# Kernel tuning notes

Hardware: AMD Instinct MI355X
Metric: run time of the kernel (lower is better)

Reference implementation:

```python
import jax, jax.numpy as jnp
import numpy as np

B, N, DIM_IN, DIM_OUT, CHEB_K, EMBED_DIM = 64, 2048, 64, 64, 3, 10


def setup_inputs() -> dict:
    key = jax.random.key(0)
    k1, k2, k3, k4 = jax.random.split(key, 4)
    x = jax.random.normal(k1, (B, N, DIM_IN), dtype=jnp.float32)
    node_embeddings = jax.random.normal(k2, (N, EMBED_DIM), dtype=jnp.float32)
    # xavier-normal-like init for the pools
    w_std = (2.0 / (EMBED_DIM * CHEB_K * DIM_IN + DIM_OUT)) ** 0.5
    b_std = (2.0 / (EMBED_DIM + DIM_OUT)) ** 0.5
    weights_pool = jax.random.normal(k3, (EMBED_DIM, CHEB_K, DIM_IN, DIM_OUT), dtype=jnp.float32) * w_std
    bias_pool = jax.random.normal(k4, (EMBED_DIM, DIM_OUT), dtype=jnp.float32) * b_std
    return {"x": x, "node_embeddings": node_embeddings,
            "weights_pool": weights_pool, "bias_pool": bias_pool,
            "cheb_k": CHEB_K}


def reference(x, node_embeddings, weights_pool, bias_pool, cheb_k):
    n = node_embeddings.shape[0]
    # adaptive adjacency: softmax(relu(E E^T)) over neighbors
    supports = jax.nn.softmax(jax.nn.relu(node_embeddings @ node_embeddings.T), axis=1)
    # Chebyshev polynomial supports: T0 = I, T1 = A, Tk = 2 A T_{k-1} - T_{k-2}
    support_set = [jnp.eye(n, dtype=supports.dtype), supports]
    for _ in range(2, cheb_k):
        support_set.append(2.0 * supports @ support_set[-1] - support_set[-2])
    supports_k = jnp.stack(support_set, axis=0)  # [K, N, N]
    # per-node weights and bias synthesized from node embeddings
    weights = jnp.einsum('nd,dkio->nkio', node_embeddings, weights_pool)  # [N, K, I, O]
    bias = node_embeddings @ bias_pool                                    # [N, O]
    # graph convolution
    x_g = jnp.einsum('knm,bmc->bnkc', supports_k, x)                      # [B, N, K, I]
    out = jnp.einsum('bnki,nkio->bno', x_g, weights) + bias               # [B, N, O]
    return out
```

## Files before the change

### kernel.cpp

```cpp
#include <hip/hip_runtime.h>

#define NN 2048
#define BB 64
#define CC 64
#define ED 10
#define KK 3
#define JJ (BB * CC)

typedef unsigned short ushort_t;
typedef __attribute__((ext_vector_type(8))) short short8;
typedef __attribute__((ext_vector_type(4))) float f32x4;

typedef const __attribute__((address_space(1))) unsigned* gptr_t;
typedef __attribute__((address_space(3))) unsigned* lptr_t;

static __device__ __forceinline__ ushort_t f2bf(float f) {
    union { float f; unsigned u; } x{f};
    unsigned r = x.u + 0x7FFF + ((x.u >> 16) & 1);
    return (ushort_t)(r >> 16);
}
static __device__ __forceinline__ float bf2f(ushort_t h) {
    union { unsigned u; float f; } x;
    x.u = ((unsigned)h) << 16;
    return x.f;
}

__global__ __launch_bounds__(256) void supports_kernel(const float* __restrict__ E,
                                                       ushort_t* __restrict__ Ab) {
    const int n = blockIdx.x;
    const int tid = threadIdx.x;

    float en[ED];
#pragma unroll
    for (int d = 0; d < ED; ++d) en[d] = E[n * ED + d];

    float sv[NN / 256];
    float lmax = 0.0f;
#pragma unroll
    for (int j = 0; j < NN / 256; ++j) {
        const int m = tid + j * 256;
        const float* Em = E + m * ED;
        float dot = 0.0f;
#pragma unroll
        for (int d = 0; d < ED; ++d) dot += en[d] * Em[d];
        float s = fmaxf(dot, 0.0f);
        sv[j] = s;
        lmax = fmaxf(lmax, s);
    }

    __shared__ float smax[4];
    __shared__ float ssum[4];
#pragma unroll
    for (int off = 32; off > 0; off >>= 1) lmax = fmaxf(lmax, __shfl_down(lmax, off, 64));
    if ((tid & 63) == 0) smax[tid >> 6] = lmax;
    __syncthreads();
    const float bmax = fmaxf(fmaxf(smax[0], smax[1]), fmaxf(smax[2], smax[3]));

    float lsum = 0.0f;
#pragma unroll
    for (int j = 0; j < NN / 256; ++j) {
        sv[j] = __expf(sv[j] - bmax);
        lsum += sv[j];
    }
#pragma unroll
    for (int off = 32; off > 0; off >>= 1) lsum += __shfl_down(lsum, off, 64);
    if ((tid & 63) == 0) ssum[tid >> 6] = lsum;
    __syncthreads();
    const float inv = 1.0f / (ssum[0] + ssum[1] + ssum[2] + ssum[3]);

#pragma unroll
    for (int j = 0; j < NN / 256; ++j) {
        Ab[(size_t)n * NN + tid + j * 256] = f2bf(sv[j] * inv);
    }
}

__global__ __launch_bounds__(256) void transpose_kernel(const float* __restrict__ x,
                                                        ushort_t* __restrict__ xT,
                                                        ushort_t* __restrict__ xN) {
    const int n0 = blockIdx.x * 64;
    const int b = blockIdx.y;
    const int tid = threadIdx.x;

    __shared__ float tb[64][68];

#pragma unroll
    for (int l = 0; l < 4; ++l) {
        const int idx = tid + l * 256;
        const int nn = idx >> 4;
        const int c4 = (idx & 15) << 2;
        const float4 v = *(const float4*)(x + ((size_t)b * NN + n0 + nn) * CC + c4);
        tb[c4 + 0][nn] = v.x;
        tb[c4 + 1][nn] = v.y;
        tb[c4 + 2][nn] = v.z;
        tb[c4 + 3][nn] = v.w;
    }
    __syncthreads();

#pragma unroll
    for (int l = 0; l < 2; ++l) {
        const int idx = tid + l * 256;
        const int c = idx >> 3;
        const int ch = (idx & 7) << 3;
        ushort_t pack[8];
#pragma unroll
        for (int e = 0; e < 8; ++e) pack[e] = f2bf(tb[c][ch + e]);
        *(float4*)(xT + (size_t)(b * 64 + c) * NN + n0 + ch) = *(float4*)pack;
    }
#pragma unroll
    for (int l = 0; l < 2; ++l) {
        const int idx = tid + l * 256;
        const int nn = idx >> 3;
        const int cg = (idx & 7) << 3;
        ushort_t pack[8];
#pragma unroll
        for (int e = 0; e < 8; ++e) pack[e] = f2bf(tb[cg + e][nn]);
        *(float4*)(xN + (size_t)(n0 + nn) * JJ + b * 64 + cg) = *(float4*)pack;
    }
}

__global__ __launch_bounds__(256) void wprep_kernel(const float* __restrict__ Wp,
                                                    ushort_t* __restrict__ WpT) {
    const int dk = blockIdx.x;
    const int tid = threadIdx.x;
    const float* src = Wp + (size_t)dk * CC * CC;

    __shared__ float tb[64][68];

#pragma unroll
    for (int l = 0; l < 4; ++l) {
        const int idx = tid + l * 256;
        const int i = idx >> 4;
        const int o4 = (idx & 15) << 2;
        const float4 v = *(const float4*)(src + i * CC + o4);
        tb[o4 + 0][i] = v.x;
        tb[o4 + 1][i] = v.y;
        tb[o4 + 2][i] = v.z;
        tb[o4 + 3][i] = v.w;
    }
    __syncthreads();

#pragma unroll
    for (int l = 0; l < 2; ++l) {
        const int idx = tid + l * 256;
        const int o = idx >> 3;
        const int ic = (idx & 7) << 3;
        ushort_t pack[8];
#pragma unroll
        for (int e = 0; e < 8; ++e) pack[e] = f2bf(tb[o][ic + e]);
        *(float4*)(WpT + (size_t)dk * CC * CC + o * CC + ic) = *(float4*)pack;
    }
}

template <int MODE>
__global__ __launch_bounds__(256) void gemm_nt(const ushort_t* __restrict__ A,
                                               const ushort_t* __restrict__ Bt,
                                               const ushort_t* __restrict__ Zn,
                                               ushort_t* __restrict__ Ct,
                                               ushort_t* __restrict__ Cn) {
    const int j0 = blockIdx.x * 128;
    const int m0 = blockIdx.y * 128;
    const int tid = threadIdx.x;
    const int lane = tid & 63;
    const int l16 = lane & 15;
    const int quad = lane >> 4;
    const int w = tid >> 6;
    const int wm = (w >> 1) * 64;
    const int wj = (w & 1) * 64;
    const int lr = lane >> 3;
    const int lc = lane & 7;
    const int swz = lc ^ lr;

    __shared__ ushort_t As[128 * 64];
    __shared__ ushort_t Bs[128 * 64];

    f32x4 acc[4][4];
#pragma unroll
    for (int mi = 0; mi < 4; ++mi)
#pragma unroll
        for (int ji = 0; ji < 4; ++ji) acc[mi][ji] = (f32x4){0.f, 0.f, 0.f, 0.f};

    for (int k0 = 0; k0 < NN; k0 += 64) {
#pragma unroll
        for (int inst = 0; inst < 4; ++inst) {
            const int rbase = w * 32 + inst * 8;
            const int row = rbase + lr;
            __builtin_amdgcn_global_load_lds(
                (gptr_t)(A + (size_t)(m0 + row) * NN + k0 + swz * 8),
                (lptr_t)&As[rbase * 64], 16, 0, 0);
            __builtin_amdgcn_global_load_lds(
                (gptr_t)(Bt + (size_t)(j0 + row) * NN + k0 + swz * 8),
                (lptr_t)&Bs[rbase * 64], 16, 0, 0);
        }
        __syncthreads();

#pragma unroll
        for (int ks = 0; ks < 64; ks += 32) {
            const int qb = (ks >> 3) + quad;
            short8 av[4], bv[4];
#pragma unroll
            for (int mi = 0; mi < 4; ++mi) {
                const int rA = wm + mi * 16 + l16;
                av[mi] = *(const short8*)&As[rA * 64 + ((qb ^ (rA & 7)) << 3)];
            }
#pragma unroll
            for (int ji = 0; ji < 4; ++ji) {
                const int rB = wj + ji * 16 + l16;
                bv[ji] = *(const short8*)&Bs[rB * 64 + ((qb ^ (rB & 7)) << 3)];
            }
#pragma unroll
            for (int mi = 0; mi < 4; ++mi)
#pragma unroll
                for (int ji = 0; ji < 4; ++ji)
                    acc[mi][ji] = __builtin_amdgcn_mfma_f32_16x16x32_bf16(
                        av[mi], bv[ji], acc[mi][ji], 0, 0, 0);
        }
        __syncthreads();
    }

#pragma unroll
    for (int mi = 0; mi < 4; ++mi) {
#pragma unroll
        for (int ji = 0; ji < 4; ++ji) {
            const int j = j0 + wj + ji * 16 + l16;
            const int mb = m0 + wm + mi * 16 + quad * 4;
            if (MODE == 0) {
                ushort_t o[4];
#pragma unroll
                for (int r = 0; r < 4; ++r) o[r] = f2bf(acc[mi][ji][r]);
                *(unsigned long long*)(Ct + (size_t)j * NN + mb) = *(unsigned long long*)o;
#pragma unroll
                for (int r = 0; r < 4; ++r) Cn[(size_t)(mb + r) * JJ + j] = o[r];
            } else {
#pragma unroll
                for (int r = 0; r < 4; ++r) {
                    const float z = bf2f(Zn[(size_t)(mb + r) * JJ + j]);
                    Cn[(size_t)(mb + r) * JJ + j] = f2bf(2.0f * acc[mi][ji][r] - z);
                }
            }
        }
    }
}

#define XLD 200
__global__ __launch_bounds__(256) void out_kernel(const float* __restrict__ E,
                                                  const ushort_t* __restrict__ WpT,
                                                  const float* __restrict__ bp,
                                                  const ushort_t* __restrict__ xN,
                                                  const ushort_t* __restrict__ y1N,
                                                  const ushort_t* __restrict__ y2N,
                                                  float* __restrict__ out) {
    const int n = blockIdx.x;
    const int tid = threadIdx.x;

    __shared__ ushort_t xg[BB * XLD];
    __shared__ ushort_t Wt[CC * XLD];
    __shared__ float en_s[ED];
    __shared__ float bias_s[CC];

    if (tid < ED) en_s[tid] = E[n * ED + tid];
    __syncthreads();

    float en[ED];
#pragma unroll
    for (int d = 0; d < ED; ++d) en[d] = en_s[d];

    if (tid < CC) {
        float bsum = 0.0f;
#pragma unroll
        for (int d = 0; d < ED; ++d) bsum += en[d] * bp[d * CC + tid];
        bias_s[tid] = bsum;
    }

#pragma unroll
    for (int k = 0; k < KK; ++k) {
        const ushort_t* src = (k == 0) ? xN : (k == 1) ? y1N : y2N;
        const float4* srow = (const float4*)(src + (size_t)n * JJ);
        for (int idx = tid; idx < JJ / 8; idx += 256) {
            *(float4*)&xg[(idx >> 3) * XLD + k * 64 + ((idx & 7) << 3)] = srow[idx];
        }
    }

    for (int t = tid; t < CC * 24; t += 256) {
        const int o = t / 24;
        const int kc = t % 24;
        const int k = kc >> 3;
        const int ic = (kc & 7) << 3;
        float s[8];
#pragma unroll
        for (int e = 0; e < 8; ++e) s[e] = 0.0f;
#pragma unroll
        for (int d = 0; d < ED; ++d) {
            const float4 wv4 = *(const float4*)(WpT + ((size_t)(d * KK + k) * CC + o) * CC + ic);
            const ushort_t* wp = (const ushort_t*)&wv4;
#pragma unroll
            for (int e = 0; e < 8; ++e) s[e] += en[d] * bf2f(wp[e]);
        }
        ushort_t pack[8];
#pragma unroll
        for (int e = 0; e < 8; ++e) pack[e] = f2bf(s[e]);
        *(float4*)&Wt[o * XLD + k * 64 + ic] = *(float4*)pack;
    }
    __syncthreads();

    const int lane = tid & 63;
    const int l16 = lane & 15;
    const int quad = lane >> 4;
    const int bm = (tid >> 6) * 16;

    f32x4 acc[4];
#pragma unroll
    for (int ji = 0; ji < 4; ++ji) acc[ji] = (f32x4){0.f, 0.f, 0.f, 0.f};

#pragma unroll
    for (int kc = 0; kc < 6; ++kc) {
        const short8 av = *(const short8*)&xg[(bm + l16) * XLD + kc * 32 + quad * 8];
#pragma unroll
        for (int ji = 0; ji < 4; ++ji) {
            const short8 bv = *(const short8*)&Wt[(ji * 16 + l16) * XLD + kc * 32 + quad * 8];
            acc[ji] = __builtin_amdgcn_mfma_f32_16x16x32_bf16(av, bv, acc[ji], 0, 0, 0);
        }
    }

#pragma unroll
    for (int ji = 0; ji < 4; ++ji) {
        const int o = ji * 16 + l16;
        const float bo = bias_s[o];
#pragma unroll
        for (int r = 0; r < 4; ++r) {
            const int b = bm + quad * 4 + r;
            out[((size_t)b * NN + n) * CC + o] = acc[ji][r] + bo;
        }
    }
}
#undef XLD

extern "C" void kernel_launch(void* const* d_in, const int* in_sizes, int n_in,
                              void* d_out, int out_size, void* d_ws, size_t ws_size,
                              hipStream_t stream) {
    const float* x  = (const float*)d_in[0];
    const float* E  = (const float*)d_in[1];
    const float* Wp = (const float*)d_in[2];
    const float* bp = (const float*)d_in[3];

    ushort_t* Ab  = (ushort_t*)d_ws;
    ushort_t* xT  = Ab + (size_t)NN * NN;
    ushort_t* xN  = xT + (size_t)JJ * NN;
    ushort_t* y1T = xN + (size_t)NN * JJ;
    ushort_t* y1N = y1T + (size_t)JJ * NN;
    ushort_t* y2N = y1N + (size_t)NN * JJ;
    ushort_t* WpT = y2N + (size_t)NN * JJ;
    float* out = (float*)d_out;

    supports_kernel<<<NN, 256, 0, stream>>>(E, Ab);
    transpose_kernel<<<dim3(NN / 64, BB), 256, 0, stream>>>(x, xT, xN);
    wprep_kernel<<<ED * KK, 256, 0, stream>>>(Wp, WpT);
    gemm_nt<0><<<dim3(JJ / 128, NN / 128), 256, 0, stream>>>(Ab, xT, nullptr, y1T, y1N);
    gemm_nt<1><<<dim3(JJ / 128, NN / 128), 256, 0, stream>>>(Ab, y1T, xN, nullptr, y2N);
    out_kernel<<<NN, 256, 0, stream>>>(E, WpT, bp, xN, y1N, y2N, out);
}
```

Measured before the change: 221.5 us.

## Double-buffer GEMM LDS tiles and precompute per-node weights in separate kernel

The Chebyshev GEMM now double-buffers its A/B tiles in LDS, issuing the next k-tile's global_load_lds before computing on the current one, with a single barrier per iteration. The per-node weight synthesis moves out of out_kernel into a new wall_kernel that handles 4 nodes per block, reusing each loaded weight-pool vector across those nodes. Results are written into the now-free Ab workspace region, processed in two halves to fit. This doubles GEMM LDS use, which may lower occupancy, and adds two launches plus a round trip through global memory for the synthesized weights.

```diff
diff --git a/kernel.cpp b/kernel.cpp
--- a/kernel.cpp
+++ b/kernel.cpp
@@ -6,6 +6,7 @@
 #define ED 10
 #define KK 3
 #define JJ (BB * CC)
+#define WROW (KK * CC * CC)
 
 typedef unsigned short ushort_t;
 typedef __attribute__((ext_vector_type(8))) short short8;
@@ -151,6 +152,51 @@
     }
 }
 
+#define WNPB 4
+__global__ __launch_bounds__(256) void wall_kernel(const float* __restrict__ E,
+                                                   const ushort_t* __restrict__ WpT,
+                                                   ushort_t* __restrict__ Wall,
+                                                   int n_base) {
+    const int n0 = n_base + blockIdx.x * WNPB;
+    const int tid = threadIdx.x;
+
+    __shared__ float es[WNPB][ED];
+    if (tid < WNPB * ED) es[tid / ED][tid % ED] = E[(size_t)(n0 + tid / ED) * ED + tid % ED];
+    __syncthreads();
+
+#pragma unroll
+    for (int c = 0; c < 6; ++c) {
+        const int t = c * 256 + tid;
+        const int k = t >> 9;
+        const int off = (t & 511) << 3;
+        float vals[ED][8];
+#pragma unroll
+        for (int d = 0; d < ED; ++d) {
+            const float4 p = *(const float4*)(WpT + (size_t)(d * KK + k) * CC * CC + off);
+            const ushort_t* pp = (const ushort_t*)&p;
+#pragma unroll
+            for (int e = 0; e < 8; ++e) vals[d][e] = bf2f(pp[e]);
+        }
+#pragma unroll
+        for (int nl = 0; nl < WNPB; ++nl) {
+            float acc[8];
+#pragma unroll
+            for (int e = 0; e < 8; ++e) acc[e] = 0.0f;
+#pragma unroll
+            for (int d = 0; d < ED; ++d) {
+                const float ed = es[nl][d];
+#pragma unroll
+                for (int e = 0; e < 8; ++e) acc[e] += ed * vals[d][e];
+            }
+            ushort_t pk[8];
+#pragma unroll
+            for (int e = 0; e < 8; ++e) pk[e] = f2bf(acc[e]);
+            *(float4*)(Wall + (size_t)(blockIdx.x * WNPB + nl) * WROW + (size_t)t * 8) =
+                *(float4*)pk;
+        }
+    }
+}
+
 template <int MODE>
 __global__ __launch_bounds__(256) void gemm_nt(const ushort_t* __restrict__ A,
                                                const ushort_t* __restrict__ Bt,
@@ -170,8 +216,8 @@
     const int lc = lane & 7;
     const int swz = lc ^ lr;
 
-    __shared__ ushort_t As[128 * 64];
-    __shared__ ushort_t Bs[128 * 64];
+    __shared__ ushort_t As[2][128 * 64];
+    __shared__ ushort_t Bs[2][128 * 64];
 
     f32x4 acc[4][4];
 #pragma unroll
@@ -179,19 +225,36 @@
 #pragma unroll
         for (int ji = 0; ji < 4; ++ji) acc[mi][ji] = (f32x4){0.f, 0.f, 0.f, 0.f};
 
-    for (int k0 = 0; k0 < NN; k0 += 64) {
-#pragma unroll
-        for (int inst = 0; inst < 4; ++inst) {
-            const int rbase = w * 32 + inst * 8;
-            const int row = rbase + lr;
-            __builtin_amdgcn_global_load_lds(
-                (gptr_t)(A + (size_t)(m0 + row) * NN + k0 + swz * 8),
-                (lptr_t)&As[rbase * 64], 16, 0, 0);
-            __builtin_amdgcn_global_load_lds(
-                (gptr_t)(Bt + (size_t)(j0 + row) * NN + k0 + swz * 8),
-                (lptr_t)&Bs[rbase * 64], 16, 0, 0);
-        }
+#pragma unroll
+    for (int inst = 0; inst < 4; ++inst) {
+        const int rbase = w * 32 + inst * 8;
+        const int row = rbase + lr;
+        __builtin_amdgcn_global_load_lds(
+            (gptr_t)(A + (size_t)(m0 + row) * NN + swz * 8),
+            (lptr_t)&As[0][rbase * 64], 16, 0, 0);
+        __builtin_amdgcn_global_load_lds(
+            (gptr_t)(Bt + (size_t)(j0 + row) * NN + swz * 8),
+            (lptr_t)&Bs[0][rbase * 64], 16, 0, 0);
+    }
+
+    for (int it = 0; it < NN / 64; ++it) {
+        const int cur = it & 1;
         __syncthreads();
+
+        if (it + 1 < NN / 64) {
+            const int k0 = (it + 1) * 64;
+#pragma unroll
+            for (int inst = 0; inst < 4; ++inst) {
+                const int rbase = w * 32 + inst * 8;
+                const int row = rbase + lr;
+                __builtin_amdgcn_global_load_lds(
+                    (gptr_t)(A + (size_t)(m0 + row) * NN + k0 + swz * 8),
+                    (lptr_t)&As[1 - cur][rbase * 64], 16, 0, 0);
+                __builtin_amdgcn_global_load_lds(
+                    (gptr_t)(Bt + (size_t)(j0 + row) * NN + k0 + swz * 8),
+                    (lptr_t)&Bs[1 - cur][rbase * 64], 16, 0, 0);
+            }
+        }
 
 #pragma unroll
         for (int ks = 0; ks < 64; ks += 32) {
@@ -200,12 +263,12 @@
 #pragma unroll
             for (int mi = 0; mi < 4; ++mi) {
                 const int rA = wm + mi * 16 + l16;
-                av[mi] = *(const short8*)&As[rA * 64 + ((qb ^ (rA & 7)) << 3)];
+                av[mi] = *(const short8*)&As[cur][rA * 64 + ((qb ^ (rA & 7)) << 3)];
             }
 #pragma unroll
             for (int ji = 0; ji < 4; ++ji) {
                 const int rB = wj + ji * 16 + l16;
-                bv[ji] = *(const short8*)&Bs[rB * 64 + ((qb ^ (rB & 7)) << 3)];
+                bv[ji] = *(const short8*)&Bs[cur][rB * 64 + ((qb ^ (rB & 7)) << 3)];
             }
 #pragma unroll
             for (int mi = 0; mi < 4; ++mi)
@@ -214,7 +277,6 @@
                     acc[mi][ji] = __builtin_amdgcn_mfma_f32_16x16x32_bf16(
                         av[mi], bv[ji], acc[mi][ji], 0, 0, 0);
         }
-        __syncthreads();
     }
 
 #pragma unroll
@@ -243,31 +305,24 @@
 
 #define XLD 200
 __global__ __launch_bounds__(256) void out_kernel(const float* __restrict__ E,
-                                                  const ushort_t* __restrict__ WpT,
+                                                  const ushort_t* __restrict__ Wall,
                                                   const float* __restrict__ bp,
                                                   const ushort_t* __restrict__ xN,
                                                   const ushort_t* __restrict__ y1N,
                                                   const ushort_t* __restrict__ y2N,
-                                                  float* __restrict__ out) {
-    const int n = blockIdx.x;
+                                                  float* __restrict__ out,
+                                                  int n_base) {
+    const int n = n_base + blockIdx.x;
     const int tid = threadIdx.x;
 
     __shared__ ushort_t xg[BB * XLD];
     __shared__ ushort_t Wt[CC * XLD];
-    __shared__ float en_s[ED];
     __shared__ float bias_s[CC];
-
-    if (tid < ED) en_s[tid] = E[n * ED + tid];
-    __syncthreads();
-
-    float en[ED];
-#pragma unroll
-    for (int d = 0; d < ED; ++d) en[d] = en_s[d];
 
     if (tid < CC) {
         float bsum = 0.0f;
 #pragma unroll
-        for (int d = 0; d < ED; ++d) bsum += en[d] * bp[d * CC + tid];
+        for (int d = 0; d < ED; ++d) bsum += E[(size_t)n * ED + d] * bp[d * CC + tid];
         bias_s[tid] = bsum;
     }
 
@@ -279,26 +334,14 @@
             *(float4*)&xg[(idx >> 3) * XLD + k * 64 + ((idx & 7) << 3)] = srow[idx];
         }
     }
-
-    for (int t = tid; t < CC * 24; t += 256) {
-        const int o = t / 24;
-        const int kc = t % 24;
-        const int k = kc >> 3;
-        const int ic = (kc & 7) << 3;
-        float s[8];
-#pragma unroll
-        for (int e = 0; e < 8; ++e) s[e] = 0.0f;
-#pragma unroll
-        for (int d = 0; d < ED; ++d) {
-            const float4 wv4 = *(const float4*)(WpT + ((size_t)(d * KK + k) * CC + o) * CC + ic);
-            const ushort_t* wp = (const ushort_t*)&wv4;
-#pragma unroll
-            for (int e = 0; e < 8; ++e) s[e] += en[d] * bf2f(wp[e]);
-        }
-        ushort_t pack[8];
-#pragma unroll
-        for (int e = 0; e < 8; ++e) pack[e] = f2bf(s[e]);
-        *(float4*)&Wt[o * XLD + k * 64 + ic] = *(float4*)pack;
+    {
+        const float4* wrow = (const float4*)(Wall + (size_t)blockIdx.x * WROW);
+        for (int t = tid; t < WROW / 8; t += 256) {
+            const int k = t >> 9;
+            const int o = (t & 511) >> 3;
+            const int ic = (t & 7) << 3;
+            *(float4*)&Wt[o * XLD + k * 64 + ic] = wrow[t];
+        }
     }
     __syncthreads();
 
@@ -342,19 +385,28 @@
     const float* Wp = (const float*)d_in[2];
     const float* bp = (const float*)d_in[3];
 
-    ushort_t* Ab  = (ushort_t*)d_ws;
+    const size_t MB = 1024 * 1024 / 2;
+    ushort_t* base = (ushort_t*)d_ws;
+    ushort_t* WpT  = base;
+    ushort_t* xN   = base + (size_t)(256 * 1024) / 2 * 2;
+    xN  = base + 131072;
+    ushort_t* y1N = xN + (size_t)NN * JJ;
+    ushort_t* y2N = y1N + (size_t)NN * JJ;
+    ushort_t* Ab  = y2N + (size_t)NN * JJ;
     ushort_t* xT  = Ab + (size_t)NN * NN;
-    ushort_t* xN  = xT + (size_t)JJ * NN;
-    ushort_t* y1T = xN + (size_t)NN * JJ;
-    ushort_t* y1N = y1T + (size_t)JJ * NN;
-    ushort_t* y2N = y1N + (size_t)NN * JJ;
-    ushort_t* WpT = y2N + (size_t)NN * JJ;
+    ushort_t* y1T = xT + (size_t)JJ * NN;
+    ushort_t* Wall = Ab;
     float* out = (float*)d_out;
+    (void)MB;
 
     supports_kernel<<<NN, 256, 0, stream>>>(E, Ab);
     transpose_kernel<<<dim3(NN / 64, BB), 256, 0, stream>>>(x, xT, xN);
     wprep_kernel<<<ED * KK, 256, 0, stream>>>(Wp, WpT);
     gemm_nt<0><<<dim3(JJ / 128, NN / 128), 256, 0, stream>>>(Ab, xT, nullptr, y1T, y1N);
     gemm_nt<1><<<dim3(JJ / 128, NN / 128), 256, 0, stream>>>(Ab, y1T, xN, nullptr, y2N);
-    out_kernel<<<NN, 256, 0, stream>>>(E, WpT, bp, xN, y1N, y2N, out);
-}
+    const int NH = NN / 2;
+    wall_kernel<<<NH / WNPB, 256, 0, stream>>>(E, WpT, Wall, 0);
+    out_kernel<<<NH, 256, 0, stream>>>(E, Wall, bp, xN, y1N, y2N, out, 0);
+    wall_kernel<<<NH / WNPB, 256, 0, stream>>>(E, WpT, Wall, NH);
+    out_kernel<<<NH, 256, 0, stream>>>(E, Wall, bp, xN, y1N, y2N, out, NH);
+}
```

Measured after the change: 253.1 us. 1.14x slower.

## Double-buffer GEMM LDS tiles and merge prep kernels into one launch

Applied to the files above, without the earlier changes.

The GEMM main loop now uses two LDS buffers per operand. Global-to-LDS loads for the next K tile are issued before the MFMAs on the current tile, and one barrier per iteration is dropped. The softmax-supports, x transpose and weight-pool prep kernels are merged into a single launch with block-index dispatch, which cuts launch overhead and lets the independent prep work run concurrently. LDS use per GEMM block doubles to 64 KB, which may reduce occupancy. The single barrier per iteration relies on the load-to-LDS wait ordering being correct.

```diff
diff --git a/kernel.cpp b/kernel.cpp
--- a/kernel.cpp
+++ b/kernel.cpp
@@ -25,129 +25,125 @@
     return x.f;
 }
 
-__global__ __launch_bounds__(256) void supports_kernel(const float* __restrict__ E,
-                                                       ushort_t* __restrict__ Ab) {
-    const int n = blockIdx.x;
+__global__ __launch_bounds__(256) void prep_kernel(const float* __restrict__ E,
+                                                   const float* __restrict__ x,
+                                                   const float* __restrict__ Wp,
+                                                   ushort_t* __restrict__ Ab,
+                                                   ushort_t* __restrict__ xT,
+                                                   ushort_t* __restrict__ xN,
+                                                   ushort_t* __restrict__ WpT) {
+    const int bid = blockIdx.x;
     const int tid = threadIdx.x;
 
-    float en[ED];
-#pragma unroll
-    for (int d = 0; d < ED; ++d) en[d] = E[n * ED + d];
-
-    float sv[NN / 256];
-    float lmax = 0.0f;
-#pragma unroll
-    for (int j = 0; j < NN / 256; ++j) {
-        const int m = tid + j * 256;
-        const float* Em = E + m * ED;
-        float dot = 0.0f;
-#pragma unroll
-        for (int d = 0; d < ED; ++d) dot += en[d] * Em[d];
-        float s = fmaxf(dot, 0.0f);
-        sv[j] = s;
-        lmax = fmaxf(lmax, s);
-    }
-
-    __shared__ float smax[4];
-    __shared__ float ssum[4];
-#pragma unroll
-    for (int off = 32; off > 0; off >>= 1) lmax = fmaxf(lmax, __shfl_down(lmax, off, 64));
-    if ((tid & 63) == 0) smax[tid >> 6] = lmax;
-    __syncthreads();
-    const float bmax = fmaxf(fmaxf(smax[0], smax[1]), fmaxf(smax[2], smax[3]));
-
-    float lsum = 0.0f;
-#pragma unroll
-    for (int j = 0; j < NN / 256; ++j) {
-        sv[j] = __expf(sv[j] - bmax);
-        lsum += sv[j];
-    }
-#pragma unroll
-    for (int off = 32; off > 0; off >>= 1) lsum += __shfl_down(lsum, off, 64);
-    if ((tid & 63) == 0) ssum[tid >> 6] = lsum;
-    __syncthreads();
-    const float inv = 1.0f / (ssum[0] + ssum[1] + ssum[2] + ssum[3]);
-
-#pragma unroll
-    for (int j = 0; j < NN / 256; ++j) {
-        Ab[(size_t)n * NN + tid + j * 256] = f2bf(sv[j] * inv);
-    }
-}
-
-__global__ __launch_bounds__(256) void transpose_kernel(const float* __restrict__ x,
-                                                        ushort_t* __restrict__ xT,
-                                                        ushort_t* __restrict__ xN) {
-    const int n0 = blockIdx.x * 64;
-    const int b = blockIdx.y;
-    const int tid = threadIdx.x;
-
     __shared__ float tb[64][68];
-
-#pragma unroll
-    for (int l = 0; l < 4; ++l) {
-        const int idx = tid + l * 256;
-        const int nn = idx >> 4;
-        const int c4 = (idx & 15) << 2;
-        const float4 v = *(const float4*)(x + ((size_t)b * NN + n0 + nn) * CC + c4);
-        tb[c4 + 0][nn] = v.x;
-        tb[c4 + 1][nn] = v.y;
-        tb[c4 + 2][nn] = v.z;
-        tb[c4 + 3][nn] = v.w;
-    }
-    __syncthreads();
-
-#pragma unroll
-    for (int l = 0; l < 2; ++l) {
-        const int idx = tid + l * 256;
-        const int c = idx >> 3;
-        const int ch = (idx & 7) << 3;
-        ushort_t pack[8];
-#pragma unroll
-        for (int e = 0; e < 8; ++e) pack[e] = f2bf(tb[c][ch + e]);
-        *(float4*)(xT + (size_t)(b * 64 + c) * NN + n0 + ch) = *(float4*)pack;
-    }
-#pragma unroll
-    for (int l = 0; l < 2; ++l) {
-        const int idx = tid + l * 256;
-        const int nn = idx >> 3;
-        const int cg = (idx & 7) << 3;
-        ushort_t pack[8];
-#pragma unroll
-        for (int e = 0; e < 8; ++e) pack[e] = f2bf(tb[cg + e][nn]);
-        *(float4*)(xN + (size_t)(n0 + nn) * JJ + b * 64 + cg) = *(float4*)pack;
-    }
-}
-
-__global__ __launch_bounds__(256) void wprep_kernel(const float* __restrict__ Wp,
-                                                    ushort_t* __restrict__ WpT) {
-    const int dk = blockIdx.x;
-    const int tid = threadIdx.x;
-    const float* src = Wp + (size_t)dk * CC * CC;
-
-    __shared__ float tb[64][68];
-
-#pragma unroll
-    for (int l = 0; l < 4; ++l) {
-        const int idx = tid + l * 256;
-        const int i = idx >> 4;
-        const int o4 = (idx & 15) << 2;
-        const float4 v = *(const float4*)(src + i * CC + o4);
-        tb[o4 + 0][i] = v.x;
-        tb[o4 + 1][i] = v.y;
-        tb[o4 + 2][i] = v.z;
-        tb[o4 + 3][i] = v.w;
-    }
-    __syncthreads();
-
-#pragma unroll
-    for (int l = 0; l < 2; ++l) {
-        const int idx = tid + l * 256;
-        const int o = idx >> 3;
-        const int ic = (idx & 7) << 3;
-        ushort_t pack[8];
-#pragma unroll
-        for (int e = 0; e < 8; ++e) pack[e] = f2bf(tb[o][ic + e]);
-        *(float4*)(WpT + (size_t)dk * CC * CC + o * CC + ic) = *(float4*)pack;
+    __shared__ float red[8];
+
+    if (bid < NN) {
+        const int n = bid;
+        float en[ED];
+#pragma unroll
+        for (int d = 0; d < ED; ++d) en[d] = E[n * ED + d];
+
+        float sv[NN / 256];
+        float lmax = 0.0f;
+#pragma unroll
+        for (int j = 0; j < NN / 256; ++j) {
+            const int m = tid + j * 256;
+            const float* Em = E + m * ED;
+            float dot = 0.0f;
+#pragma unroll
+            for (int d = 0; d < ED; ++d) dot += en[d] * Em[d];
+            float s = fmaxf(dot, 0.0f);
+            sv[j] = s;
+            lmax = fmaxf(lmax, s);
+        }
+#pragma unroll
+        for (int off = 32; off > 0; off >>= 1) lmax = fmaxf(lmax, __shfl_down(lmax, off, 64));
+        if ((tid & 63) == 0) red[tid >> 6] = lmax;
+        __syncthreads();
+        const float bmax = fmaxf(fmaxf(red[0], red[1]), fmaxf(red[2], red[3]));
+
+        float lsum = 0.0f;
+#pragma unroll
+        for (int j = 0; j < NN / 256; ++j) {
+            sv[j] = __expf(sv[j] - bmax);
+            lsum += sv[j];
+        }
+#pragma unroll
+        for (int off = 32; off > 0; off >>= 1) lsum += __shfl_down(lsum, off, 64);
+        if ((tid & 63) == 0) red[4 + (tid >> 6)] = lsum;
+        __syncthreads();
+        const float inv = 1.0f / (red[4] + red[5] + red[6] + red[7]);
+
+#pragma unroll
+        for (int j = 0; j < NN / 256; ++j) {
+            Ab[(size_t)n * NN + tid + j * 256] = f2bf(sv[j] * inv);
+        }
+    } else if (bid < 2 * NN) {
+        const int t = bid - NN;
+        const int n0 = (t & 31) * 64;
+        const int b = t >> 5;
+
+#pragma unroll
+        for (int l = 0; l < 4; ++l) {
+            const int idx = tid + l * 256;
+            const int nn = idx >> 4;
+            const int c4 = (idx & 15) << 2;
+            const float4 v = *(const float4*)(x + ((size_t)b * NN + n0 + nn) * CC + c4);
+            tb[c4 + 0][nn] = v.x;
+            tb[c4 + 1][nn] = v.y;
+            tb[c4 + 2][nn] = v.z;
+            tb[c4 + 3][nn] = v.w;
+        }
+        __syncthreads();
+
+#pragma unroll
+        for (int l = 0; l < 2; ++l) {
+            const int idx = tid + l * 256;
+            const int c = idx >> 3;
+            const int ch = (idx & 7) << 3;
+            ushort_t pack[8];
+#pragma unroll
+            for (int e = 0; e < 8; ++e) pack[e] = f2bf(tb[c][ch + e]);
+            *(float4*)(xT + (size_t)(b * 64 + c) * NN + n0 + ch) = *(float4*)pack;
+        }
+#pragma unroll
+        for (int l = 0; l < 2; ++l) {
+            const int idx = tid + l * 256;
+            const int nn = idx >> 3;
+            const int cg = (idx & 7) << 3;
+            ushort_t pack[8];
+#pragma unroll
+            for (int e = 0; e < 8; ++e) pack[e] = f2bf(tb[cg + e][nn]);
+            *(float4*)(xN + (size_t)(n0 + nn) * JJ + b * 64 + cg) = *(float4*)pack;
+        }
+    } else {
+        const int dk = bid - 2 * NN;
+        const float* src = Wp + (size_t)dk * CC * CC;
+
+#pragma unroll
+        for (int l = 0; l < 4; ++l) {
+            const int idx = tid + l * 256;
+            const int i = idx >> 4;
+            const int o4 = (idx & 15) << 2;
+            const float4 v = *(const float4*)(src + i * CC + o4);
+            tb[o4 + 0][i] = v.x;
+            tb[o4 + 1][i] = v.y;
+            tb[o4 + 2][i] = v.z;
+            tb[o4 + 3][i] = v.w;
+        }
+        __syncthreads();
+
+#pragma unroll
+        for (int l = 0; l < 2; ++l) {
+            const int idx = tid + l * 256;
+            const int o = idx >> 3;
+            const int ic = (idx & 7) << 3;
+            ushort_t pack[8];
+#pragma unroll
+            for (int e = 0; e < 8; ++e) pack[e] = f2bf(tb[o][ic + e]);
+            *(float4*)(WpT + (size_t)dk * CC * CC + o * CC + ic) = *(float4*)pack;
+        }
     }
 }
 
@@ -170,8 +166,8 @@
     const int lc = lane & 7;
     const int swz = lc ^ lr;
 
-    __shared__ ushort_t As[128 * 64];
-    __shared__ ushort_t Bs[128 * 64];
+    __shared__ ushort_t As[2][128 * 64];
+    __shared__ ushort_t Bs[2][128 * 64];
 
     f32x4 acc[4][4];
 #pragma unroll
@@ -179,19 +175,36 @@
 #pragma unroll
         for (int ji = 0; ji < 4; ++ji) acc[mi][ji] = (f32x4){0.f, 0.f, 0.f, 0.f};
 
-    for (int k0 = 0; k0 < NN; k0 += 64) {
-#pragma unroll
-        for (int inst = 0; inst < 4; ++inst) {
-            const int rbase = w * 32 + inst * 8;
-            const int row = rbase + lr;
-            __builtin_amdgcn_global_load_lds(
-                (gptr_t)(A + (size_t)(m0 + row) * NN + k0 + swz * 8),
-                (lptr_t)&As[rbase * 64], 16, 0, 0);
-            __builtin_amdgcn_global_load_lds(
-                (gptr_t)(Bt + (size_t)(j0 + row) * NN + k0 + swz * 8),
-                (lptr_t)&Bs[rbase * 64], 16, 0, 0);
-        }
-        __syncthreads();
+#pragma unroll
+    for (int inst = 0; inst < 4; ++inst) {
+        const int rbase = w * 32 + inst * 8;
+        const int row = rbase + lr;
+        __builtin_amdgcn_global_load_lds(
+            (gptr_t)(A + (size_t)(m0 + row) * NN + swz * 8),
+            (lptr_t)&As[0][rbase * 64], 16, 0, 0);
+        __builtin_amdgcn_global_load_lds(
+            (gptr_t)(Bt + (size_t)(j0 + row) * NN + swz * 8),
+            (lptr_t)&Bs[0][rbase * 64], 16, 0, 0);
+    }
+
+    for (int it = 0; it < NN / 64; ++it) {
+        const int cur = it & 1;
+        __syncthreads();
+
+        if (it + 1 < NN / 64) {
+            const int k0 = (it + 1) * 64;
+#pragma unroll
+            for (int inst = 0; inst < 4; ++inst) {
+                const int rbase = w * 32 + inst * 8;
+                const int row = rbase + lr;
+                __builtin_amdgcn_global_load_lds(
+                    (gptr_t)(A + (size_t)(m0 + row) * NN + k0 + swz * 8),
+                    (lptr_t)&As[1 - cur][rbase * 64], 16, 0, 0);
+                __builtin_amdgcn_global_load_lds(
+                    (gptr_t)(Bt + (size_t)(j0 + row) * NN + k0 + swz * 8),
+                    (lptr_t)&Bs[1 - cur][rbase * 64], 16, 0, 0);
+            }
+        }
 
 #pragma unroll
         for (int ks = 0; ks < 64; ks += 32) {
@@ -200,12 +213,12 @@
 #pragma unroll
             for (int mi = 0; mi < 4; ++mi) {
                 const int rA = wm + mi * 16 + l16;
-                av[mi] = *(const short8*)&As[rA * 64 + ((qb ^ (rA & 7)) << 3)];
+                av[mi] = *(const short8*)&As[cur][rA * 64 + ((qb ^ (rA & 7)) << 3)];
             }
 #pragma unroll
             for (int ji = 0; ji < 4; ++ji) {
                 const int rB = wj + ji * 16 + l16;
-                bv[ji] = *(const short8*)&Bs[rB * 64 + ((qb ^ (rB & 7)) << 3)];
+                bv[ji] = *(const short8*)&Bs[cur][rB * 64 + ((qb ^ (rB & 7)) << 3)];
             }
 #pragma unroll
             for (int mi = 0; mi < 4; ++mi)
@@ -214,7 +227,6 @@
                     acc[mi][ji] = __builtin_amdgcn_mfma_f32_16x16x32_bf16(
                         av[mi], bv[ji], acc[mi][ji], 0, 0, 0);
         }
-        __syncthreads();
     }
 
 #pragma unroll
@@ -351,9 +363,7 @@
     ushort_t* WpT = y2N + (size_t)NN * JJ;
     float* out = (float*)d_out;
 
-    supports_kernel<<<NN, 256, 0, stream>>>(E, Ab);
-    transpose_kernel<<<dim3(NN / 64, BB), 256, 0, stream>>>(x, xT, xN);
-    wprep_kernel<<<ED * KK, 256, 0, stream>>>(Wp, WpT);
+    prep_kernel<<<2 * NN + ED * KK, 256, 0, stream>>>(E, x, Wp, Ab, xT, xN, WpT);
     gemm_nt<0><<<dim3(JJ / 128, NN / 128), 256, 0, stream>>>(Ab, xT, nullptr, y1T, y1N);
     gemm_nt<1><<<dim3(JJ / 128, NN / 128), 256, 0, stream>>>(Ab, y1T, xN, nullptr, y2N);
     out_kernel<<<NN, 256, 0, stream>>>(E, WpT, bp, xN, y1N, y2N, out);
```

Result: no change. 218.1 us (-1.6%).
